# Kernel tuning notes

Hardware: AMD Instinct MI355X
Metric: run time of the kernel (lower is better)

## Reference

```python
import jax, jax.numpy as jnp
import numpy as np

D_MODEL, WIN, STRIDE, NHEAD, HEAD_DIM, FFN_H = 96, 16, 8, 6, 16, 192
INNER = NHEAD * HEAD_DIM
EPS = 1e-5


def _ln(x, g, b):
    m = jnp.mean(x, axis=-1, keepdims=True)
    v = jnp.mean((x - m) ** 2, axis=-1, keepdims=True)
    return (x - m) / jnp.sqrt(v + EPS) * g + b


def setup_inputs() -> dict:
    key = jax.random.key(0)
    ks = jax.random.split(key, 16)
    B, L, D = 32, 8192, D_MODEL
    sd = lambda n: 1.0 / np.sqrt(n)
    return {
        "x": jax.random.normal(ks[0], (B, L, D), jnp.float32),
        "ln1_g": jnp.ones((D,), jnp.float32),
        "ln1_b": jnp.zeros((D,), jnp.float32),
        "qkv_w": jax.random.normal(ks[1], (D, 3 * INNER), jnp.float32) * sd(D),
        "qkv_b": jnp.zeros((3 * INNER,), jnp.float32),
        "out_w": jax.random.normal(ks[2], (INNER, D), jnp.float32) * sd(INNER),
        "out_b": jnp.zeros((D,), jnp.float32),
        "ln2_g": jnp.ones((D,), jnp.float32),
        "ln2_b": jnp.zeros((D,), jnp.float32),
        "ffn_w1": jax.random.normal(ks[3], (D, FFN_H), jnp.float32) * sd(D),
        "ffn_b1": jnp.zeros((FFN_H,), jnp.float32),
        "ffn_w2": jax.random.normal(ks[4], (FFN_H, D), jnp.float32) * sd(FFN_H),
        "ffn_b2": jnp.zeros((D,), jnp.float32),
        "pln_g": jnp.ones((D,), jnp.float32),
        "pln_b": jnp.zeros((D,), jnp.float32),
    }


def reference(x, ln1_g, ln1_b, qkv_w, qkv_b, out_w, out_b,
              ln2_g, ln2_b, ffn_w1, ffn_b1, ffn_w2, ffn_b2, pln_g, pln_b):
    B, L, D = x.shape
    w, s = WIN, STRIDE
    num_win = 1 + (L - w) // s  # all windows fit since (num_win-1)*s + w <= L
    idx = jnp.arange(num_win)[:, None] * s + jnp.arange(w)[None, :]  # [N, w]

    seg = x[:, idx]  # [B, N, w, D] gather of overlapping windows

    # --- pre-LN attention block, vectorized over all windows ---
    h = _ln(seg, ln1_g, ln1_b)
    qkv = h @ qkv_w + qkv_b  # [B, N, w, 3*INNER]
    q, k, v = jnp.split(qkv, 3, axis=-1)
    shp = (B, num_win, w, NHEAD, HEAD_DIM)
    q, k, v = q.reshape(shp), k.reshape(shp), v.reshape(shp)
    scores = jnp.einsum('bnqhd,bnkhd->bnhqk', q, k) / np.sqrt(HEAD_DIM).astype(np.float32)
    causal = jnp.tril(jnp.ones((w, w), bool))
    scores = jnp.where(causal, scores, -jnp.inf)
    attn = jax.nn.softmax(scores, axis=-1)
    o = jnp.einsum('bnhqk,bnkhd->bnqhd', attn, v).reshape(B, num_win, w, INNER)
    o = o @ out_w + out_b
    h = seg + o

    # --- FFN block ---
    h2 = _ln(h, ln2_g, ln2_b)
    h = h + (jax.nn.gelu(h2 @ ffn_w1 + ffn_b1) @ ffn_w2 + ffn_b2)
    h = _ln(h, pln_g, pln_b)

    # --- overlap-add average ---
    out = jnp.zeros((B, L, D), x.dtype).at[:, idx].add(h)
    cnt = jnp.zeros((L,), x.dtype).at[idx.reshape(-1)].add(1.0)
    return out / jnp.maximum(cnt, 1.0)[None, :, None]
```

## Files before the change

kernel.cpp:

```cpp
#include <hip/hip_runtime.h>
#include <hip/hip_bf16.h>

typedef __attribute__((ext_vector_type(8))) short short8;
typedef __attribute__((ext_vector_type(4))) float f32x4;
typedef __attribute__((ext_vector_type(4))) unsigned u32x4;

#define LDS_BYTES 40960
#define SH   104
#define SU   52
#define KOFF 3328
#define VOFF 6656
#define F1S  200
#define F1SU 100

#if __has_builtin(__builtin_amdgcn_cvt_pk_bf16_f32)
typedef __attribute__((ext_vector_type(2))) __bf16 bf16x2;
__device__ __forceinline__ unsigned pk2bf(float a, float b){
  bf16x2 v = __builtin_amdgcn_cvt_pk_bf16_f32(a, b);
  return __builtin_bit_cast(unsigned, v);
}
__device__ __forceinline__ unsigned short f2bf(float x){
  bf16x2 v = __builtin_amdgcn_cvt_pk_bf16_f32(x, x);
  return (unsigned short)(__builtin_bit_cast(unsigned, v) & 0xFFFFu);
}
#else
__device__ __forceinline__ unsigned short f2bf(float x){
  unsigned u = __float_as_uint(x);
  u += 0x7FFFu + ((u >> 16) & 1u);
  return (unsigned short)(u >> 16);
}
__device__ __forceinline__ unsigned pk2bf(float a, float b){
  return (unsigned)f2bf(a) | ((unsigned)f2bf(b) << 16);
}
#endif

#if __has_builtin(__builtin_amdgcn_rcpf)
__device__ __forceinline__ float fast_rcp(float x){ return __builtin_amdgcn_rcpf(x); }
#else
__device__ __forceinline__ float fast_rcp(float x){ return 1.f/x; }
#endif
#if __has_builtin(__builtin_amdgcn_rsqf)
__device__ __forceinline__ float fast_rsq(float x){ return __builtin_amdgcn_rsqf(x); }
#else
__device__ __forceinline__ float fast_rsq(float x){ return rsqrtf(x); }
#endif
#if __has_builtin(__builtin_amdgcn_exp2f)
__device__ __forceinline__ float fast_ex2(float x){ return __builtin_amdgcn_exp2f(x); }
#else
__device__ __forceinline__ float fast_ex2(float x){ return exp2f(x); }
#endif

__device__ __forceinline__ float bflo(unsigned u){ return __uint_as_float(u << 16); }
__device__ __forceinline__ float bfhi(unsigned u){ return __uint_as_float(u & 0xFFFF0000u); }
__device__ __forceinline__ float bf1(unsigned short h){ return __uint_as_float(((unsigned)h) << 16); }

__global__ void zero_stripes(float* __restrict__ out){
  int k = blockIdx.x;
  int b = blockIdx.y;
  int t = threadIdx.x;
  int tok = 24*k + (t / 24);
  f32x4 z = {0.f, 0.f, 0.f, 0.f};
  *(f32x4*)(out + ((size_t)b*8192 + tok)*96 + 4*(t % 24)) = z;
}

__global__ void pack_weights(const float* __restrict__ qkv_w, const float* __restrict__ out_w,
                             const float* __restrict__ ffn_w1, const float* __restrict__ ffn_w2,
                             short8* __restrict__ wsv){
  int f = blockIdx.x, lane = threadIdx.x;
  const float* W; int N, nt, kf;
  if (f < 54)      { W = qkv_w;  N = 288; nt = f/3;        kf = f%3; }
  else if (f < 72) { int i=f-54;  W = out_w;  N = 96;  nt = i/3; kf = i%3; }
  else if (f < 108){ int i=f-72;  W = ffn_w1; N = 192; nt = i/3; kf = i%3; }
  else             { int i=f-108; W = ffn_w2; N = 96;  nt = i/6; kf = i%6; }
  int n = lane & 15, kq = lane >> 4;
  short8 v;
#pragma unroll
  for (int j = 0; j < 8; ++j){
    int k = kf*32 + kq*8 + j;
    v[j] = (short)f2bf(W[(size_t)k * N + nt*16 + n]);
  }
  wsv[f*64 + lane] = v;
}

__global__ __launch_bounds__(512, 8)
void fused_block(const float* __restrict__ x,
                 const float* __restrict__ ln1_g, const float* __restrict__ ln1_b,
                 const float* __restrict__ qkv_b,
                 const float* __restrict__ out_b,
                 const float* __restrict__ ln2_g, const float* __restrict__ ln2_b,
                 const float* __restrict__ ffn_b1, const float* __restrict__ ffn_b2,
                 const float* __restrict__ pln_g, const float* __restrict__ pln_b,
                 const short8* __restrict__ wsv,
                 float* __restrict__ out)
{
  __shared__ __align__(16) char smem[LDS_BYTES];
  unsigned short* hres  = (unsigned short*)smem;
  unsigned*       hresU = (unsigned*)smem;
  unsigned short* buf1  = (unsigned short*)(smem + 9984);
  unsigned*       buf1U = (unsigned*)(smem + 9984);
  unsigned short* buf2  = (unsigned short*)(smem + 19968);
  unsigned*       buf2U = (unsigned*)(smem + 19968);

  const int tid  = threadIdx.x;
  const int wave = tid >> 6, lane = tid & 63;
  const int lm   = lane & 15, quad = lane >> 4;
  __builtin_assume(wave >= 0 && wave < 8);
  __builtin_assume(lm >= 0 && lm < 16);
  __builtin_assume(quad >= 0 && quad < 4);
  const int g = blockIdx.x, b = blockIdx.y;
  const int t0 = 24 * g;
  const size_t xbase = ((size_t)b * 8192 + t0) * 96;
  const short8* wl = wsv + lane;

  {
    const int mt = wave & 1, p = wave >> 1;
    __builtin_assume(p >= 0 && p < 4);
    const int row = 16*mt + lm;
    const float* xr = x + xbase + (size_t)row*96 + quad*8;
    float v0[8], v1[8], v2[8];
    {
      f32x4 a = *(const f32x4*)(xr);       f32x4 c = *(const f32x4*)(xr + 4);
#pragma unroll
      for (int j = 0; j < 4; ++j){ v0[j] = a[j]; v0[4+j] = c[j]; }
    }
    {
      f32x4 a = *(const f32x4*)(xr + 32);  f32x4 c = *(const f32x4*)(xr + 36);
#pragma unroll
      for (int j = 0; j < 4; ++j){ v1[j] = a[j]; v1[4+j] = c[j]; }
    }
    {
      f32x4 a = *(const f32x4*)(xr + 64);  f32x4 c = *(const f32x4*)(xr + 68);
#pragma unroll
      for (int j = 0; j < 4; ++j){ v2[j] = a[j]; v2[4+j] = c[j]; }
    }
    float s = 0.f, q2 = 0.f;
#pragma unroll
    for (int j = 0; j < 8; ++j){
      s += v0[j] + v1[j] + v2[j];
      q2 += v0[j]*v0[j] + v1[j]*v1[j] + v2[j]*v2[j];
    }
    s  += __shfl_xor(s, 16);  q2 += __shfl_xor(q2, 16);
    s  += __shfl_xor(s, 32);  q2 += __shfl_xor(q2, 32);
    float mean = s * (1.f/96.f);
    float rstd = fast_rsq(q2 * (1.f/96.f) - mean*mean + 1e-5f);

    short8 h0, h1, h2;
    auto mkfrag = [&](const float* vv, int kf)->short8{
      const float* gp = ln1_g + kf*32 + quad*8;
      const float* bp = ln1_b + kf*32 + quad*8;
      f32x4 ga = *(const f32x4*)(gp), gb = *(const f32x4*)(gp + 4);
      f32x4 ba = *(const f32x4*)(bp), bb = *(const f32x4*)(bp + 4);
      u32x4 hu;
      hu[0] = pk2bf((vv[0]-mean)*rstd*ga[0]+ba[0], (vv[1]-mean)*rstd*ga[1]+ba[1]);
      hu[1] = pk2bf((vv[2]-mean)*rstd*ga[2]+ba[2], (vv[3]-mean)*rstd*ga[3]+ba[3]);
      hu[2] = pk2bf((vv[4]-mean)*rstd*gb[0]+bb[0], (vv[5]-mean)*rstd*gb[1]+bb[1]);
      hu[3] = pk2bf((vv[6]-mean)*rstd*gb[2]+bb[2], (vv[7]-mean)*rstd*gb[3]+bb[3]);
      return __builtin_bit_cast(short8, hu);
    };
    h0 = mkfrag(v0, 0); h1 = mkfrag(v1, 1); h2 = mkfrag(v2, 2);

    auto qkv_tile = [&](int nt){
      if (nt < 12){
        f32x4 acc0 = *(const f32x4*)(qkv_b + nt*16 + quad*4);
        f32x4 acc1 = {0.f,0.f,0.f,0.f};
        acc0 = __builtin_amdgcn_mfma_f32_16x16x32_bf16(wl[(nt*3+0)*64], h0, acc0, 0, 0, 0);
        acc1 = __builtin_amdgcn_mfma_f32_16x16x32_bf16(wl[(nt*3+1)*64], h1, acc1, 0, 0, 0);
        acc0 = __builtin_amdgcn_mfma_f32_16x16x32_bf16(wl[(nt*3+2)*64], h2, acc0, 0, 0, 0);
        unsigned idx = (nt < 6)
          ? (unsigned)(row*SU + nt*8 + quad*2)
          : (unsigned)((KOFF>>1) + row*SU + (nt-6)*8 + quad*2);
        buf2U[idx]     = pk2bf(acc0[0]+acc1[0], acc0[1]+acc1[1]);
        buf2U[idx + 1] = pk2bf(acc0[2]+acc1[2], acc0[3]+acc1[3]);
      } else {
        int col = nt*16 + lm;
        float bias = qkv_b[col];
        f32x4 acc0 = {bias, bias, bias, bias};
        f32x4 acc1 = {0.f,0.f,0.f,0.f};
        acc0 = __builtin_amdgcn_mfma_f32_16x16x32_bf16(h0, wl[(nt*3+0)*64], acc0, 0, 0, 0);
        acc1 = __builtin_amdgcn_mfma_f32_16x16x32_bf16(h1, wl[(nt*3+1)*64], acc1, 0, 0, 0);
        acc0 = __builtin_amdgcn_mfma_f32_16x16x32_bf16(h2, wl[(nt*3+2)*64], acc0, 0, 0, 0);
        int d2 = col - 192;
        int w0 = (VOFF >> 1) + d2*20 + 8*mt + 2*quad;
        buf2U[w0]     = pk2bf(acc0[0]+acc1[0], acc0[1]+acc1[1]);
        buf2U[w0 + 1] = pk2bf(acc0[2]+acc1[2], acc0[3]+acc1[3]);
      }
    };
#pragma unroll
    for (int i = 0; i < 4; ++i) qkv_tile(p + 4*i);
    if (p < 2) qkv_tile(p + 16);
  }
  __syncthreads();

  {
    auto attn_unit = [&](int u){
      int w = u / 6, h = u - 6*(u / 6);
      short8 qa = {0,0,0,0,0,0,0,0}, ka = {0,0,0,0,0,0,0,0};
      if (quad < 2){
        qa = *(const short8*)(buf2 +        (8*w + lm)*SH + h*16 + quad*8);
        ka = *(const short8*)(buf2 + KOFF + (8*w + lm)*SH + h*16 + quad*8);
      }
      f32x4 sc = {0.f,0.f,0.f,0.f};
      sc = __builtin_amdgcn_mfma_f32_16x16x32_bf16(ka, qa, sc, 0, 0, 0);
      float p4[4]; float sum = 0.f;
#pragma unroll
      for (int r = 0; r < 4; ++r){
        int k = quad*4 + r;
        float e = fast_ex2(sc[r]*0.36067376f);
        p4[r] = (k <= lm) ? e : 0.f;
        sum += p4[r];
      }
      sum += __shfl_xor(sum, 16);
      sum += __shfl_xor(sum, 32);
      float rs = fast_rcp(sum);
      int x0 = (int)pk2bf(p4[0]*rs, p4[1]*rs);
      int x1 = (int)pk2bf(p4[2]*rs, p4[3]*rs);
      int srcA = lm + ((quad & 1) << 5);
      int e0 = __shfl(x0, srcA),      e1 = __shfl(x1, srcA);
      int e2 = __shfl(x0, srcA + 16), e3 = __shfl(x1, srcA + 16);
      short8 pa = {0,0,0,0,0,0,0,0}, va = {0,0,0,0,0,0,0,0};
      if (quad < 2){
        u32x4 t = {(unsigned)e0, (unsigned)e1, (unsigned)e2, (unsigned)e3};
        pa = __builtin_bit_cast(short8, t);
        va = *(const short8*)(buf2 + VOFF + (h*16 + lm)*40 + 8*w + quad*8);
      }
      f32x4 oc = {0.f,0.f,0.f,0.f};
      oc = __builtin_amdgcn_mfma_f32_16x16x32_bf16(va, pa, oc, 0, 0, 0);
      unsigned ob = (w*16 + lm)*SU + h*8 + quad*2;
      buf1U[ob]     = pk2bf(oc[0], oc[1]);
      buf1U[ob + 1] = pk2bf(oc[2], oc[3]);
    };
    attn_unit(wave);
    attn_unit(wave + 8);
    if (wave < 2) attn_unit(wave + 16);
  }
  __syncthreads();

  {
    auto oproj_tile = [&](int tile){
      int w = tile / 6, nt = tile - 6*(tile / 6);
      f32x4 acc0 = *(const f32x4*)(out_b + nt*16 + quad*4);
      f32x4 acc1 = {0.f,0.f,0.f,0.f};
      const unsigned short* arow = buf1 + (w*16 + lm)*SH + quad*8;
      short8 a0 = *(const short8*)(arow);
      short8 a1 = *(const short8*)(arow + 32);
      short8 a2 = *(const short8*)(arow + 64);
      acc0 = __builtin_amdgcn_mfma_f32_16x16x32_bf16(wl[(54 + nt*3 + 0)*64], a0, acc0, 0, 0, 0);
      acc1 = __builtin_amdgcn_mfma_f32_16x16x32_bf16(wl[(54 + nt*3 + 1)*64], a1, acc1, 0, 0, 0);
      acc0 = __builtin_amdgcn_mfma_f32_16x16x32_bf16(wl[(54 + nt*3 + 2)*64], a2, acc0, 0, 0, 0);
      f32x4 xr = *(const f32x4*)(x + xbase + (size_t)(8*w + lm)*96 + nt*16 + quad*4);
      unsigned idx = (w*16 + lm)*SU + nt*8 + quad*2;
      hresU[idx]     = pk2bf(acc0[0]+acc1[0]+xr[0], acc0[1]+acc1[1]+xr[1]);
      hresU[idx + 1] = pk2bf(acc0[2]+acc1[2]+xr[2], acc0[3]+acc1[3]+xr[3]);
    };
    oproj_tile(wave);
    oproj_tile(wave + 8);
    if (wave < 2) oproj_tile(wave + 16);
  }
  __syncthreads();

  if (wave < 6){
    const int mt = wave >> 1, ntb = (wave & 1)*6;
    const int row = 16*mt + lm;
    const unsigned short* hr = hres + row*SH + quad*8;
    short8 r0 = *(const short8*)(hr);
    short8 r1 = *(const short8*)(hr + 32);
    short8 r2 = *(const short8*)(hr + 64);
    u32x4 c0 = __builtin_bit_cast(u32x4, r0);
    u32x4 c1 = __builtin_bit_cast(u32x4, r1);
    u32x4 c2 = __builtin_bit_cast(u32x4, r2);
    float s = 0.f, q2 = 0.f;
#pragma unroll
    for (int t = 0; t < 4; ++t){
      float a0 = bflo(c0[t]), a1 = bfhi(c0[t]);
      float a2 = bflo(c1[t]), a3 = bfhi(c1[t]);
      float a4 = bflo(c2[t]), a5 = bfhi(c2[t]);
      s  += a0+a1+a2+a3+a4+a5;
      q2 += a0*a0+a1*a1+a2*a2+a3*a3+a4*a4+a5*a5;
    }
    s  += __shfl_xor(s, 16);  q2 += __shfl_xor(q2, 16);
    s  += __shfl_xor(s, 32);  q2 += __shfl_xor(q2, 32);
    float mean = s * (1.f/96.f);
    float rstd = fast_rsq(q2 * (1.f/96.f) - mean*mean + 1e-5f);

    short8 a0f, a1f, a2f;
    auto mkfrag2 = [&](u32x4 c, int kf)->short8{
      const float* gp = ln2_g + kf*32 + quad*8;
      const float* bp = ln2_b + kf*32 + quad*8;
      f32x4 ga = *(const f32x4*)(gp), gb = *(const f32x4*)(gp + 4);
      f32x4 ba = *(const f32x4*)(bp), bb = *(const f32x4*)(bp + 4);
      u32x4 hu;
      hu[0] = pk2bf((bflo(c[0])-mean)*rstd*ga[0]+ba[0], (bfhi(c[0])-mean)*rstd*ga[1]+ba[1]);
      hu[1] = pk2bf((bflo(c[1])-mean)*rstd*ga[2]+ba[2], (bfhi(c[1])-mean)*rstd*ga[3]+ba[3]);
      hu[2] = pk2bf((bflo(c[2])-mean)*rstd*gb[0]+bb[0], (bfhi(c[2])-mean)*rstd*gb[1]+bb[1]);
      hu[3] = pk2bf((bflo(c[3])-mean)*rstd*gb[2]+bb[2], (bfhi(c[3])-mean)*rstd*gb[3]+bb[3]);
      return __builtin_bit_cast(short8, hu);
    };
    a0f = mkfrag2(c0, 0); a1f = mkfrag2(c1, 1); a2f = mkfrag2(c2, 2);

#pragma unroll
    for (int i = 0; i < 6; ++i){
      int nt = ntb + i;
      f32x4 acc0 = *(const f32x4*)(ffn_b1 + nt*16 + quad*4);
      f32x4 acc1 = {0.f,0.f,0.f,0.f};
      acc0 = __builtin_amdgcn_mfma_f32_16x16x32_bf16(wl[(72 + nt*3 + 0)*64], a0f, acc0, 0, 0, 0);
      acc1 = __builtin_amdgcn_mfma_f32_16x16x32_bf16(wl[(72 + nt*3 + 1)*64], a1f, acc1, 0, 0, 0);
      acc0 = __builtin_amdgcn_mfma_f32_16x16x32_bf16(wl[(72 + nt*3 + 2)*64], a2f, acc0, 0, 0, 0);
      float gl[4];
#pragma unroll
      for (int r = 0; r < 4; ++r){
        float uu = acc0[r] + acc1[r];
        float z = -2.3022081f * (uu + 0.044715f * uu*uu*uu);
        float e = fast_ex2(z);
        gl[r] = uu * fast_rcp(1.f + e);
      }
      unsigned idx = (mt*16 + lm)*F1SU + nt*8 + quad*2;
      buf2U[idx]     = pk2bf(gl[0], gl[1]);
      buf2U[idx + 1] = pk2bf(gl[2], gl[3]);
    }
  }
  __syncthreads();

  {
    auto ffn2_tile = [&](int tile){
      int mt = tile / 6, nt = tile - 6*(tile / 6);
      const unsigned short* frow = buf2 + (mt*16 + lm)*F1S + quad*8;
      short8 f0 = *(const short8*)(frow);
      short8 f1 = *(const short8*)(frow + 32);
      short8 f2 = *(const short8*)(frow + 64);
      short8 f3 = *(const short8*)(frow + 96);
      short8 f4 = *(const short8*)(frow + 128);
      short8 f5 = *(const short8*)(frow + 160);
      f32x4 acc0 = *(const f32x4*)(ffn_b2 + nt*16 + quad*4);
      f32x4 acc1 = {0.f,0.f,0.f,0.f};
      acc0 = __builtin_amdgcn_mfma_f32_16x16x32_bf16(wl[(108 + nt*6 + 0)*64], f0, acc0, 0, 0, 0);
      acc1 = __builtin_amdgcn_mfma_f32_16x16x32_bf16(wl[(108 + nt*6 + 1)*64], f1, acc1, 0, 0, 0);
      acc0 = __builtin_amdgcn_mfma_f32_16x16x32_bf16(wl[(108 + nt*6 + 2)*64], f2, acc0, 0, 0, 0);
      acc1 = __builtin_amdgcn_mfma_f32_16x16x32_bf16(wl[(108 + nt*6 + 3)*64], f3, acc1, 0, 0, 0);
      acc0 = __builtin_amdgcn_mfma_f32_16x16x32_bf16(wl[(108 + nt*6 + 4)*64], f4, acc0, 0, 0, 0);
      acc1 = __builtin_amdgcn_mfma_f32_16x16x32_bf16(wl[(108 + nt*6 + 5)*64], f5, acc1, 0, 0, 0);
      unsigned idx = (mt*16 + lm)*SU + nt*8 + quad*2;
      unsigned u0 = hresU[idx], u1 = hresU[idx + 1];
      hresU[idx]     = pk2bf(bflo(u0)+acc0[0]+acc1[0], bfhi(u0)+acc0[1]+acc1[1]);
      hresU[idx + 1] = pk2bf(bflo(u1)+acc0[2]+acc1[2], bfhi(u1)+acc0[3]+acc1[3]);
    };
    ffn2_tile(wave);
    ffn2_tile(wave + 8);
    if (wave < 2) ffn2_tile(wave + 16);
  }
  __syncthreads();

  {
    const int i = tid >> 4, c0 = tid & 15;
    const int l = t0 + i;
    const size_t obase = ((size_t)b * 8192 + l) * 96;
    int rowA, rowB = -1;
    if (i < 8)       rowA = i;
    else if (i < 16){ rowA = i;            rowB = 16 + (i - 8); }
    else if (i < 24){ rowA = 16 + (i - 8); rowB = 32 + (i - 16); }
    else             rowA = 32 + (i - 16);

    float g6[6], b6[6];
#pragma unroll
    for (int e = 0; e < 6; ++e){ g6[e] = pln_g[c0 + 16*e]; b6[e] = pln_b[c0 + 16*e]; }

    float yA[6];
    {
      float v[6];
#pragma unroll
      for (int e = 0; e < 6; ++e) v[e] = bf1(hres[rowA*SH + c0 + 16*e]);
      float s = 0.f, q2 = 0.f;
#pragma unroll
      for (int e = 0; e < 6; ++e){ s += v[e]; q2 += v[e]*v[e]; }
#pragma unroll
      for (int m = 1; m < 16; m <<= 1){ s += __shfl_xor(s, m, 16); q2 += __shfl_xor(q2, m, 16); }
      float mean = s * (1.f/96.f);
      float rstd = fast_rsq(q2 * (1.f/96.f) - mean*mean + 1e-5f);
#pragma unroll
      for (int e = 0; e < 6; ++e) yA[e] = (v[e]-mean)*rstd*g6[e] + b6[e];
    }
    if (rowB >= 0){
      float yB[6];
      {
        float v[6];
#pragma unroll
        for (int e = 0; e < 6; ++e) v[e] = bf1(hres[rowB*SH + c0 + 16*e]);
        float s = 0.f, q2 = 0.f;
#pragma unroll
        for (int e = 0; e < 6; ++e){ s += v[e]; q2 += v[e]*v[e]; }
#pragma unroll
        for (int m = 1; m < 16; m <<= 1){ s += __shfl_xor(s, m, 16); q2 += __shfl_xor(q2, m, 16); }
        float mean = s * (1.f/96.f);
        float rstd = fast_rsq(q2 * (1.f/96.f) - mean*mean + 1e-5f);
#pragma unroll
        for (int e = 0; e < 6; ++e) yB[e] = (v[e]-mean)*rstd*g6[e] + b6[e];
      }
#pragma unroll
      for (int e = 0; e < 6; ++e)
        out[obase + c0 + 16*e] = 0.5f * (yA[e] + yB[e]);
    } else {
      float inv = (l < 8 || l >= 8184) ? 1.0f : 0.5f;
#pragma unroll
      for (int e = 0; e < 6; ++e)
        atomicAdd(&out[obase + c0 + 16*e], yA[e] * inv);
    }
  }
}

extern "C" void kernel_launch(void* const* d_in, const int* in_sizes, int n_in,
                              void* d_out, int out_size, void* d_ws, size_t ws_size,
                              hipStream_t stream) {
  const float* x      = (const float*)d_in[0];
  const float* ln1_g  = (const float*)d_in[1];
  const float* ln1_b  = (const float*)d_in[2];
  const float* qkv_w  = (const float*)d_in[3];
  const float* qkv_b  = (const float*)d_in[4];
  const float* out_w  = (const float*)d_in[5];
  const float* out_b  = (const float*)d_in[6];
  const float* ln2_g  = (const float*)d_in[7];
  const float* ln2_b  = (const float*)d_in[8];
  const float* ffn_w1 = (const float*)d_in[9];
  const float* ffn_b1 = (const float*)d_in[10];
  const float* ffn_w2 = (const float*)d_in[11];
  const float* ffn_b2 = (const float*)d_in[12];
  const float* pln_g  = (const float*)d_in[13];
  const float* pln_b  = (const float*)d_in[14];
  float* out = (float*)d_out;
  short8* wsv = (short8*)d_ws;

  zero_stripes<<<dim3(342, 32), 192, 0, stream>>>(out);
  pack_weights<<<144, 64, 0, stream>>>(qkv_w, out_w, ffn_w1, ffn_w2, wsv);
  fused_block<<<dim3(341, 32), 512, 0, stream>>>(
      x, ln1_g, ln1_b, qkv_b, out_b, ln2_g, ln2_b, ffn_b1, ffn_b2,
      pln_g, pln_b, (const short8*)wsv, out);
}
```

Baseline: 510.2 us.

## Compute a fourth partial window per block to drop output zeroing and atomics

Each block now also handles the next block's leading window, with its second half masked off, so every token in a block's stripe is fully owned. Tokens can then be written directly with plain stores, and the separate zero-fill kernel and the atomicAdd path are removed. LN1 is staged through LDS and the LDS buffers are remapped into one region. The cost is some redundant attention, projection and FFN work on the extra window, plus extra masking logic.

```diff
diff --git a/kernel.cpp b/kernel.cpp
--- a/kernel.cpp
+++ b/kernel.cpp
@@ -10,6 +10,12 @@
 #define SU   52
 #define KOFF 3328
 #define VOFF 6656
+#define OB_S 10496
+#define OB_U 5248
+#define F1M_S 10496
+#define F1M_U 5248
+#define F1P_S 5824
+#define F1P_U 2912
 #define F1S  200
 #define F1SU 100
 
@@ -54,15 +60,6 @@
 __device__ __forceinline__ float bfhi(unsigned u){ return __uint_as_float(u & 0xFFFF0000u); }
 __device__ __forceinline__ float bf1(unsigned short h){ return __uint_as_float(((unsigned)h) << 16); }
 
-__global__ void zero_stripes(float* __restrict__ out){
-  int k = blockIdx.x;
-  int b = blockIdx.y;
-  int t = threadIdx.x;
-  int tok = 24*k + (t / 24);
-  f32x4 z = {0.f, 0.f, 0.f, 0.f};
-  *(f32x4*)(out + ((size_t)b*8192 + tok)*96 + 4*(t % 24)) = z;
-}
-
 __global__ void pack_weights(const float* __restrict__ qkv_w, const float* __restrict__ out_w,
                              const float* __restrict__ ffn_w1, const float* __restrict__ ffn_w2,
                              short8* __restrict__ wsv){
@@ -94,12 +91,8 @@
                  float* __restrict__ out)
 {
   __shared__ __align__(16) char smem[LDS_BYTES];
-  unsigned short* hres  = (unsigned short*)smem;
-  unsigned*       hresU = (unsigned*)smem;
-  unsigned short* buf1  = (unsigned short*)(smem + 9984);
-  unsigned*       buf1U = (unsigned*)(smem + 9984);
-  unsigned short* buf2  = (unsigned short*)(smem + 19968);
-  unsigned*       buf2U = (unsigned*)(smem + 19968);
+  unsigned short* sS = (unsigned short*)smem;
+  unsigned*       sU = (unsigned*)smem;
 
   const int tid  = threadIdx.x;
   const int wave = tid >> 6, lane = tid & 63;
@@ -113,52 +106,35 @@
   const short8* wl = wsv + lane;
 
   {
+    const int row = tid >> 4, j = tid & 15;
+    const float* xr = x + xbase + (size_t)row*96 + 6*j;
+    float v[6];
+#pragma unroll
+    for (int e = 0; e < 3; ++e){ float2 t = *(const float2*)(xr + 2*e); v[2*e]=t.x; v[2*e+1]=t.y; }
+    float s = 0.f, q2 = 0.f;
+#pragma unroll
+    for (int e = 0; e < 6; ++e){ s += v[e]; q2 += v[e]*v[e]; }
+#pragma unroll
+    for (int m = 1; m < 16; m <<= 1){ s += __shfl_xor(s, m, 16); q2 += __shfl_xor(q2, m, 16); }
+    float mean = s * (1.f/96.f);
+    float rstd = fast_rsq(q2 * (1.f/96.f) - mean*mean + 1e-5f);
+#pragma unroll
+    for (int e = 0; e < 3; ++e){
+      float2 gg = *(const float2*)(ln1_g + 6*j + 2*e);
+      float2 bb = *(const float2*)(ln1_b + 6*j + 2*e);
+      sU[OB_U + row*SU + 3*j + e] = pk2bf((v[2*e]-mean)*rstd*gg.x+bb.x,
+                                          (v[2*e+1]-mean)*rstd*gg.y+bb.y);
+    }
+  }
+  __syncthreads();
+
+  {
     const int mt = wave & 1, p = wave >> 1;
     __builtin_assume(p >= 0 && p < 4);
-    const int row = 16*mt + lm;
-    const float* xr = x + xbase + (size_t)row*96 + quad*8;
-    float v0[8], v1[8], v2[8];
-    {
-      f32x4 a = *(const f32x4*)(xr);       f32x4 c = *(const f32x4*)(xr + 4);
-#pragma unroll
-      for (int j = 0; j < 4; ++j){ v0[j] = a[j]; v0[4+j] = c[j]; }
-    }
-    {
-      f32x4 a = *(const f32x4*)(xr + 32);  f32x4 c = *(const f32x4*)(xr + 36);
-#pragma unroll
-      for (int j = 0; j < 4; ++j){ v1[j] = a[j]; v1[4+j] = c[j]; }
-    }
-    {
-      f32x4 a = *(const f32x4*)(xr + 64);  f32x4 c = *(const f32x4*)(xr + 68);
-#pragma unroll
-      for (int j = 0; j < 4; ++j){ v2[j] = a[j]; v2[4+j] = c[j]; }
-    }
-    float s = 0.f, q2 = 0.f;
-#pragma unroll
-    for (int j = 0; j < 8; ++j){
-      s += v0[j] + v1[j] + v2[j];
-      q2 += v0[j]*v0[j] + v1[j]*v1[j] + v2[j]*v2[j];
-    }
-    s  += __shfl_xor(s, 16);  q2 += __shfl_xor(q2, 16);
-    s  += __shfl_xor(s, 32);  q2 += __shfl_xor(q2, 32);
-    float mean = s * (1.f/96.f);
-    float rstd = fast_rsq(q2 * (1.f/96.f) - mean*mean + 1e-5f);
-
-    short8 h0, h1, h2;
-    auto mkfrag = [&](const float* vv, int kf)->short8{
-      const float* gp = ln1_g + kf*32 + quad*8;
-      const float* bp = ln1_b + kf*32 + quad*8;
-      f32x4 ga = *(const f32x4*)(gp), gb = *(const f32x4*)(gp + 4);
-      f32x4 ba = *(const f32x4*)(bp), bb = *(const f32x4*)(bp + 4);
-      u32x4 hu;
-      hu[0] = pk2bf((vv[0]-mean)*rstd*ga[0]+ba[0], (vv[1]-mean)*rstd*ga[1]+ba[1]);
-      hu[1] = pk2bf((vv[2]-mean)*rstd*ga[2]+ba[2], (vv[3]-mean)*rstd*ga[3]+ba[3]);
-      hu[2] = pk2bf((vv[4]-mean)*rstd*gb[0]+bb[0], (vv[5]-mean)*rstd*gb[1]+bb[1]);
-      hu[3] = pk2bf((vv[6]-mean)*rstd*gb[2]+bb[2], (vv[7]-mean)*rstd*gb[3]+bb[3]);
-      return __builtin_bit_cast(short8, hu);
-    };
-    h0 = mkfrag(v0, 0); h1 = mkfrag(v1, 1); h2 = mkfrag(v2, 2);
-
+    const unsigned short* arow = sS + OB_S + (16*mt + lm)*SH + quad*8;
+    short8 h0 = *(const short8*)(arow);
+    short8 h1 = *(const short8*)(arow + 32);
+    short8 h2 = *(const short8*)(arow + 64);
     auto qkv_tile = [&](int nt){
       if (nt < 12){
         f32x4 acc0 = *(const f32x4*)(qkv_b + nt*16 + quad*4);
@@ -166,11 +142,12 @@
         acc0 = __builtin_amdgcn_mfma_f32_16x16x32_bf16(wl[(nt*3+0)*64], h0, acc0, 0, 0, 0);
         acc1 = __builtin_amdgcn_mfma_f32_16x16x32_bf16(wl[(nt*3+1)*64], h1, acc1, 0, 0, 0);
         acc0 = __builtin_amdgcn_mfma_f32_16x16x32_bf16(wl[(nt*3+2)*64], h2, acc0, 0, 0, 0);
+        int row = 16*mt + lm;
         unsigned idx = (nt < 6)
           ? (unsigned)(row*SU + nt*8 + quad*2)
           : (unsigned)((KOFF>>1) + row*SU + (nt-6)*8 + quad*2);
-        buf2U[idx]     = pk2bf(acc0[0]+acc1[0], acc0[1]+acc1[1]);
-        buf2U[idx + 1] = pk2bf(acc0[2]+acc1[2], acc0[3]+acc1[3]);
+        sU[idx]     = pk2bf(acc0[0]+acc1[0], acc0[1]+acc1[1]);
+        sU[idx + 1] = pk2bf(acc0[2]+acc1[2], acc0[3]+acc1[3]);
       } else {
         int col = nt*16 + lm;
         float bias = qkv_b[col];
@@ -181,8 +158,8 @@
         acc0 = __builtin_amdgcn_mfma_f32_16x16x32_bf16(h2, wl[(nt*3+2)*64], acc0, 0, 0, 0);
         int d2 = col - 192;
         int w0 = (VOFF >> 1) + d2*20 + 8*mt + 2*quad;
-        buf2U[w0]     = pk2bf(acc0[0]+acc1[0], acc0[1]+acc1[1]);
-        buf2U[w0 + 1] = pk2bf(acc0[2]+acc1[2], acc0[3]+acc1[3]);
+        sU[w0]     = pk2bf(acc0[0]+acc1[0], acc0[1]+acc1[1]);
+        sU[w0 + 1] = pk2bf(acc0[2]+acc1[2], acc0[3]+acc1[3]);
       }
     };
 #pragma unroll
@@ -194,10 +171,11 @@
   {
     auto attn_unit = [&](int u){
       int w = u / 6, h = u - 6*(u / 6);
+      bool pref = (w == 3);
       short8 qa = {0,0,0,0,0,0,0,0}, ka = {0,0,0,0,0,0,0,0};
       if (quad < 2){
-        qa = *(const short8*)(buf2 +        (8*w + lm)*SH + h*16 + quad*8);
-        ka = *(const short8*)(buf2 + KOFF + (8*w + lm)*SH + h*16 + quad*8);
+        qa = *(const short8*)(sS +        (8*w + lm)*SH + h*16 + quad*8);
+        ka = *(const short8*)(sS + KOFF + (8*w + lm)*SH + h*16 + quad*8);
       }
       f32x4 sc = {0.f,0.f,0.f,0.f};
       sc = __builtin_amdgcn_mfma_f32_16x16x32_bf16(ka, qa, sc, 0, 0, 0);
@@ -206,12 +184,13 @@
       for (int r = 0; r < 4; ++r){
         int k = quad*4 + r;
         float e = fast_ex2(sc[r]*0.36067376f);
-        p4[r] = (k <= lm) ? e : 0.f;
+        bool ok = (k <= lm) && (!pref || (k < 8 && lm < 8));
+        p4[r] = ok ? e : 0.f;
         sum += p4[r];
       }
       sum += __shfl_xor(sum, 16);
       sum += __shfl_xor(sum, 32);
-      float rs = fast_rcp(sum);
+      float rs = fast_rcp(sum + 1e-30f);
       int x0 = (int)pk2bf(p4[0]*rs, p4[1]*rs);
       int x1 = (int)pk2bf(p4[2]*rs, p4[3]*rs);
       int srcA = lm + ((quad & 1) << 5);
@@ -221,17 +200,18 @@
       if (quad < 2){
         u32x4 t = {(unsigned)e0, (unsigned)e1, (unsigned)e2, (unsigned)e3};
         pa = __builtin_bit_cast(short8, t);
-        va = *(const short8*)(buf2 + VOFF + (h*16 + lm)*40 + 8*w + quad*8);
+        if (!(pref && quad == 1))
+          va = *(const short8*)(sS + VOFF + (h*16 + lm)*40 + 8*w + quad*8);
       }
       f32x4 oc = {0.f,0.f,0.f,0.f};
       oc = __builtin_amdgcn_mfma_f32_16x16x32_bf16(va, pa, oc, 0, 0, 0);
-      unsigned ob = (w*16 + lm)*SU + h*8 + quad*2;
-      buf1U[ob]     = pk2bf(oc[0], oc[1]);
-      buf1U[ob + 1] = pk2bf(oc[2], oc[3]);
+      unsigned ob = OB_U + (w*16 + lm)*SU + h*8 + quad*2;
+      sU[ob]     = pk2bf(oc[0], oc[1]);
+      sU[ob + 1] = pk2bf(oc[2], oc[3]);
     };
     attn_unit(wave);
     attn_unit(wave + 8);
-    if (wave < 2) attn_unit(wave + 16);
+    attn_unit(wave + 16);
   }
   __syncthreads();
 
@@ -240,34 +220,31 @@
       int w = tile / 6, nt = tile - 6*(tile / 6);
       f32x4 acc0 = *(const f32x4*)(out_b + nt*16 + quad*4);
       f32x4 acc1 = {0.f,0.f,0.f,0.f};
-      const unsigned short* arow = buf1 + (w*16 + lm)*SH + quad*8;
+      const unsigned short* arow = sS + OB_S + (w*16 + lm)*SH + quad*8;
       short8 a0 = *(const short8*)(arow);
       short8 a1 = *(const short8*)(arow + 32);
       short8 a2 = *(const short8*)(arow + 64);
       acc0 = __builtin_amdgcn_mfma_f32_16x16x32_bf16(wl[(54 + nt*3 + 0)*64], a0, acc0, 0, 0, 0);
       acc1 = __builtin_amdgcn_mfma_f32_16x16x32_bf16(wl[(54 + nt*3 + 1)*64], a1, acc1, 0, 0, 0);
       acc0 = __builtin_amdgcn_mfma_f32_16x16x32_bf16(wl[(54 + nt*3 + 2)*64], a2, acc0, 0, 0, 0);
-      f32x4 xr = *(const f32x4*)(x + xbase + (size_t)(8*w + lm)*96 + nt*16 + quad*4);
+      int xrow = (w < 3) ? (8*w + lm) : min(24 + lm, 31);
+      f32x4 xr = *(const f32x4*)(x + xbase + (size_t)xrow*96 + nt*16 + quad*4);
       unsigned idx = (w*16 + lm)*SU + nt*8 + quad*2;
-      hresU[idx]     = pk2bf(acc0[0]+acc1[0]+xr[0], acc0[1]+acc1[1]+xr[1]);
-      hresU[idx + 1] = pk2bf(acc0[2]+acc1[2]+xr[2], acc0[3]+acc1[3]+xr[3]);
+      sU[idx]     = pk2bf(acc0[0]+acc1[0]+xr[0], acc0[1]+acc1[1]+xr[1]);
+      sU[idx + 1] = pk2bf(acc0[2]+acc1[2]+xr[2], acc0[3]+acc1[3]+xr[3]);
     };
     oproj_tile(wave);
     oproj_tile(wave + 8);
-    if (wave < 2) oproj_tile(wave + 16);
-  }
-  __syncthreads();
-
-  if (wave < 6){
+    oproj_tile(wave + 16);
+  }
+  __syncthreads();
+
+  {
     const int mt = wave >> 1, ntb = (wave & 1)*6;
-    const int row = 16*mt + lm;
-    const unsigned short* hr = hres + row*SH + quad*8;
-    short8 r0 = *(const short8*)(hr);
-    short8 r1 = *(const short8*)(hr + 32);
-    short8 r2 = *(const short8*)(hr + 64);
-    u32x4 c0 = __builtin_bit_cast(u32x4, r0);
-    u32x4 c1 = __builtin_bit_cast(u32x4, r1);
-    u32x4 c2 = __builtin_bit_cast(u32x4, r2);
+    const unsigned short* hr = sS + (16*mt + lm)*SH + quad*8;
+    u32x4 c0 = __builtin_bit_cast(u32x4, *(const short8*)(hr));
+    u32x4 c1 = __builtin_bit_cast(u32x4, *(const short8*)(hr + 32));
+    u32x4 c2 = __builtin_bit_cast(u32x4, *(const short8*)(hr + 64));
     float s = 0.f, q2 = 0.f;
 #pragma unroll
     for (int t = 0; t < 4; ++t){
@@ -281,8 +258,6 @@
     s  += __shfl_xor(s, 32);  q2 += __shfl_xor(q2, 32);
     float mean = s * (1.f/96.f);
     float rstd = fast_rsq(q2 * (1.f/96.f) - mean*mean + 1e-5f);
-
-    short8 a0f, a1f, a2f;
     auto mkfrag2 = [&](u32x4 c, int kf)->short8{
       const float* gp = ln2_g + kf*32 + quad*8;
       const float* bp = ln2_b + kf*32 + quad*8;
@@ -295,8 +270,11 @@
       hu[3] = pk2bf((bflo(c[3])-mean)*rstd*gb[2]+bb[2], (bfhi(c[3])-mean)*rstd*gb[3]+bb[3]);
       return __builtin_bit_cast(short8, hu);
     };
-    a0f = mkfrag2(c0, 0); a1f = mkfrag2(c1, 1); a2f = mkfrag2(c2, 2);
-
+    short8 a0f = mkfrag2(c0, 0);
+    short8 a1f = mkfrag2(c1, 1);
+    short8 a2f = mkfrag2(c2, 2);
+    unsigned fbase = (mt < 3) ? (unsigned)(F1M_U + (mt*16 + lm)*F1SU)
+                              : (unsigned)(F1P_U + lm*F1SU);
 #pragma unroll
     for (int i = 0; i < 6; ++i){
       int nt = ntb + i;
@@ -313,17 +291,21 @@
         float e = fast_ex2(z);
         gl[r] = uu * fast_rcp(1.f + e);
       }
-      unsigned idx = (mt*16 + lm)*F1SU + nt*8 + quad*2;
-      buf2U[idx]     = pk2bf(gl[0], gl[1]);
-      buf2U[idx + 1] = pk2bf(gl[2], gl[3]);
+      unsigned idx = fbase + nt*8 + quad*2;
+      sU[idx]     = pk2bf(gl[0], gl[1]);
+      sU[idx + 1] = pk2bf(gl[2], gl[3]);
     }
   }
   __syncthreads();
 
   {
-    auto ffn2_tile = [&](int tile){
-      int mt = tile / 6, nt = tile - 6*(tile / 6);
-      const unsigned short* frow = buf2 + (mt*16 + lm)*F1S + quad*8;
+    const int mt = wave >> 1, ntb = (wave & 1)*3;
+    const unsigned short* frow = (mt < 3) ? (sS + F1M_S + (mt*16 + lm)*F1S + quad*8)
+                                          : (sS + F1P_S + lm*F1S + quad*8);
+    const bool wr = (mt < 3) | (lm < 8);
+#pragma unroll
+    for (int i = 0; i < 3; ++i){
+      int nt = ntb + i;
       short8 f0 = *(const short8*)(frow);
       short8 f1 = *(const short8*)(frow + 32);
       short8 f2 = *(const short8*)(frow + 64);
@@ -338,52 +320,39 @@
       acc1 = __builtin_amdgcn_mfma_f32_16x16x32_bf16(wl[(108 + nt*6 + 3)*64], f3, acc1, 0, 0, 0);
       acc0 = __builtin_amdgcn_mfma_f32_16x16x32_bf16(wl[(108 + nt*6 + 4)*64], f4, acc0, 0, 0, 0);
       acc1 = __builtin_amdgcn_mfma_f32_16x16x32_bf16(wl[(108 + nt*6 + 5)*64], f5, acc1, 0, 0, 0);
-      unsigned idx = (mt*16 + lm)*SU + nt*8 + quad*2;
-      unsigned u0 = hresU[idx], u1 = hresU[idx + 1];
-      hresU[idx]     = pk2bf(bflo(u0)+acc0[0]+acc1[0], bfhi(u0)+acc0[1]+acc1[1]);
-      hresU[idx + 1] = pk2bf(bflo(u1)+acc0[2]+acc1[2], bfhi(u1)+acc0[3]+acc1[3]);
-    };
-    ffn2_tile(wave);
-    ffn2_tile(wave + 8);
-    if (wave < 2) ffn2_tile(wave + 16);
+      if (wr){
+        unsigned idx = (16*mt + lm)*SU + nt*8 + quad*2;
+        unsigned u0 = sU[idx], u1 = sU[idx + 1];
+        sU[idx]     = pk2bf(bflo(u0)+acc0[0]+acc1[0], bfhi(u0)+acc0[1]+acc1[1]);
+        sU[idx + 1] = pk2bf(bflo(u1)+acc0[2]+acc1[2], bfhi(u1)+acc0[3]+acc1[3]);
+      }
+    }
   }
   __syncthreads();
 
   {
     const int i = tid >> 4, c0 = tid & 15;
-    const int l = t0 + i;
-    const size_t obase = ((size_t)b * 8192 + l) * 96;
-    int rowA, rowB = -1;
-    if (i < 8)       rowA = i;
-    else if (i < 16){ rowA = i;            rowB = 16 + (i - 8); }
-    else if (i < 24){ rowA = 16 + (i - 8); rowB = 32 + (i - 16); }
-    else             rowA = 32 + (i - 16);
-
-    float g6[6], b6[6];
-#pragma unroll
-    for (int e = 0; e < 6; ++e){ g6[e] = pln_g[c0 + 16*e]; b6[e] = pln_b[c0 + 16*e]; }
-
-    float yA[6];
-    {
-      float v[6];
-#pragma unroll
-      for (int e = 0; e < 6; ++e) v[e] = bf1(hres[rowA*SH + c0 + 16*e]);
-      float s = 0.f, q2 = 0.f;
-#pragma unroll
-      for (int e = 0; e < 6; ++e){ s += v[e]; q2 += v[e]*v[e]; }
-#pragma unroll
-      for (int m = 1; m < 16; m <<= 1){ s += __shfl_xor(s, m, 16); q2 += __shfl_xor(q2, m, 16); }
-      float mean = s * (1.f/96.f);
-      float rstd = fast_rsq(q2 * (1.f/96.f) - mean*mean + 1e-5f);
-#pragma unroll
-      for (int e = 0; e < 6; ++e) yA[e] = (v[e]-mean)*rstd*g6[e] + b6[e];
-    }
-    if (rowB >= 0){
-      float yB[6];
+    int l, rowA, rowB = -1;
+    bool active = true;
+    if (i < 24){
+      l = t0 + 8 + i;
+      rowA = 8 + i + 8*(i >> 3);
+      rowB = rowA + 8;
+      if (g == 340 && i >= 16) rowB = -1;
+    } else if (g == 0){
+      l = i - 24;  rowA = i - 24;
+    } else active = false;
+
+    if (active){
+      const size_t obase = ((size_t)b * 8192 + l) * 96;
+      float g6[6], b6[6];
+#pragma unroll
+      for (int e = 0; e < 6; ++e){ g6[e] = pln_g[c0 + 16*e]; b6[e] = pln_b[c0 + 16*e]; }
+      float yA[6];
       {
         float v[6];
 #pragma unroll
-        for (int e = 0; e < 6; ++e) v[e] = bf1(hres[rowB*SH + c0 + 16*e]);
+        for (int e = 0; e < 6; ++e) v[e] = bf1(sS[rowA*SH + c0 + 16*e]);
         float s = 0.f, q2 = 0.f;
 #pragma unroll
         for (int e = 0; e < 6; ++e){ s += v[e]; q2 += v[e]*v[e]; }
@@ -392,16 +361,32 @@
         float mean = s * (1.f/96.f);
         float rstd = fast_rsq(q2 * (1.f/96.f) - mean*mean + 1e-5f);
 #pragma unroll
-        for (int e = 0; e < 6; ++e) yB[e] = (v[e]-mean)*rstd*g6[e] + b6[e];
-      }
-#pragma unroll
-      for (int e = 0; e < 6; ++e)
-        out[obase + c0 + 16*e] = 0.5f * (yA[e] + yB[e]);
-    } else {
-      float inv = (l < 8 || l >= 8184) ? 1.0f : 0.5f;
-#pragma unroll
-      for (int e = 0; e < 6; ++e)
-        atomicAdd(&out[obase + c0 + 16*e], yA[e] * inv);
+        for (int e = 0; e < 6; ++e) yA[e] = (v[e]-mean)*rstd*g6[e] + b6[e];
+      }
+      if (rowB >= 0){
+        float yB[6];
+        {
+          float v[6];
+#pragma unroll
+          for (int e = 0; e < 6; ++e) v[e] = bf1(sS[rowB*SH + c0 + 16*e]);
+          float s = 0.f, q2 = 0.f;
+#pragma unroll
+          for (int e = 0; e < 6; ++e){ s += v[e]; q2 += v[e]*v[e]; }
+#pragma unroll
+          for (int m = 1; m < 16; m <<= 1){ s += __shfl_xor(s, m, 16); q2 += __shfl_xor(q2, m, 16); }
+          float mean = s * (1.f/96.f);
+          float rstd = fast_rsq(q2 * (1.f/96.f) - mean*mean + 1e-5f);
+#pragma unroll
+          for (int e = 0; e < 6; ++e) yB[e] = (v[e]-mean)*rstd*g6[e] + b6[e];
+        }
+#pragma unroll
+        for (int e = 0; e < 6; ++e)
+          out[obase + c0 + 16*e] = 0.5f * (yA[e] + yB[e]);
+      } else {
+#pragma unroll
+        for (int e = 0; e < 6; ++e)
+          out[obase + c0 + 16*e] = yA[e];
+      }
     }
   }
 }
@@ -427,7 +412,6 @@
   float* out = (float*)d_out;
   short8* wsv = (short8*)d_ws;
 
-  zero_stripes<<<dim3(342, 32), 192, 0, stream>>>(out);
   pack_weights<<<144, 64, 0, stream>>>(qkv_w, out_w, ffn_w1, ffn_w2, wsv);
   fused_block<<<dim3(341, 32), 512, 0, stream>>>(
       x, ln1_g, ln1_b, qkv_b, out_b, ln2_g, ln2_b, ffn_b1, ffn_b2,
```

Result: faster. 469.8 us (-7.9%).
